# Optimization experiments

Measured on AMD Instinct MI355X. Metric: run time of the kernel, lower is better.

The kernel has to match this reference:

```python
import jax, jax.numpy as jnp
import numpy as np

MASK_VALUE = -1000000.0  # matches torch sequence_mask fill value


def setup_inputs() -> dict:
    key = jax.random.key(0)
    k1, k2, k3, k4 = jax.random.split(key, 4)
    B, Tq, Tk, d = 16, 2048, 2048, 128
    queries = jax.random.normal(k1, (B, Tq, d), dtype=jnp.float32)
    keys = jax.random.normal(k2, (B, Tk, d), dtype=jnp.float32)
    values = jax.random.normal(k3, (B, Tk, d), dtype=jnp.float32)
    valid_lens = jax.random.randint(k4, (B, Tq), 0, Tk, dtype=jnp.int64)
    return {"queries": queries, "keys": keys, "values": values,
            "valid_lens": valid_lens}


def reference(queries, keys, values, valid_lens):
    d = queries.shape[-1]
    Tk = keys.shape[1]
    # scores: [B, Tq, Tk]
    scores = jnp.einsum('bqd,bkd->bqk', queries, keys) / jnp.sqrt(
        jnp.asarray(d, dtype=queries.dtype))
    # per-row length mask: position k is valid iff k < valid_lens[b, q]
    mask = jnp.arange(Tk)[None, None, :] < valid_lens[:, :, None]
    scores = jnp.where(mask, scores, jnp.asarray(MASK_VALUE, scores.dtype))
    attn = jax.nn.softmax(scores, axis=-1)
    # dropout p=0.0 -> identity
    return jnp.einsum('bqk,bkd->bqd', attn, values)
```

## Files before the change

kernel.cpp:

```cpp
#include <hip/hip_runtime.h>
#include <stdint.h>
#include <math.h>

#define NB 16
#define TQ 2048
#define TK 2048
#define DH 128
#define KT (TK / 64)
#define QB (TQ / 64)

#define QK_STR 136
#define VT_STR 72
#define P_STR  72

typedef __attribute__((ext_vector_type(8))) short bf16x8;
typedef __attribute__((ext_vector_type(4))) float f32x4;
typedef __attribute__((ext_vector_type(8))) unsigned short u16x8;

__device__ __forceinline__ unsigned short f2b(float f) {
  union { float f; uint32_t u; } v; v.f = f;
  uint32_t u = v.u;
  return (unsigned short)((u + 0x7fffu + ((u >> 16) & 1u)) >> 16);
}

__device__ __forceinline__ u16x8 cvt8(const float* p) {
  const f32x4 a = *(const f32x4*)p;
  const f32x4 b = *(const f32x4*)(p + 4);
  u16x8 o;
#pragma unroll
  for (int j = 0; j < 4; ++j) { o[j] = f2b(a[j]); o[4 + j] = f2b(b[j]); }
  return o;
}

__global__ __launch_bounds__(256) void sort_kernel(const int* __restrict__ vlen,
                                                   int* __restrict__ perm) {
  __shared__ int cnt[TK + 1];
  __shared__ int base_[TK + 1];
  __shared__ int psum[256];
  const int b = blockIdx.x;
  const int t = threadIdx.x;

  int hw = 0;
#pragma unroll
  for (int i = 0; i < 8; ++i) hw |= vlen[2 * i + 1];
  const bool is64 = (hw == 0);

  for (int i = t; i <= TK; i += 256) cnt[i] = 0;
  __syncthreads();

  int eff[8];
#pragma unroll
  for (int j = 0; j < 8; ++j) {
    const int q = j * 256 + t;
    const int idx = b * TQ + q;
    int v = is64 ? vlen[2 * idx] : vlen[idx];
    v = (v < 0) ? 0 : ((v > TK) ? TK : v);
    eff[j] = (v == 0) ? TK : v;
    atomicAdd(&cnt[eff[j]], 1);
  }
  __syncthreads();

  int loc[8]; int s = 0;
#pragma unroll
  for (int j = 0; j < 8; ++j) { loc[j] = cnt[TK - (t * 8 + j)]; s += loc[j]; }
  psum[t] = s;
  __syncthreads();
  if (t == 0) {
    int acc = 0;
    for (int i = 0; i < 256; ++i) { const int x = psum[i]; psum[i] = acc; acc += x; }
  }
  __syncthreads();
  int run = psum[t];
#pragma unroll
  for (int j = 0; j < 8; ++j) { base_[TK - (t * 8 + j)] = run; run += loc[j]; }
  __syncthreads();
#pragma unroll
  for (int j = 0; j < 8; ++j) {
    const int rank = atomicAdd(&base_[eff[j]], 1);
    perm[b * TQ + rank] = j * 256 + t;
  }
}

__global__ __launch_bounds__(256) void prep_kernel(const float* __restrict__ K,
                                                   const float* __restrict__ V,
                                                   unsigned short* __restrict__ Kb,
                                                   unsigned short* __restrict__ Vt) {
  __shared__ alignas(16) unsigned short tile[64][136];
  const int t = threadIdx.x;
  const int b = blockIdx.y;
  const int kt = blockIdx.x;
  const int k0 = kt * 64;

  const float* Ks = K + ((size_t)b * TK + k0) * DH;
  unsigned short* Kd = Kb + ((size_t)b * TK + k0) * DH;
#pragma unroll
  for (int i = 0; i < 4; ++i) {
    const int row = i * 16 + (t >> 4);
    const int c0 = (t & 15) * 8;
    *(u16x8*)(Kd + (size_t)row * DH + c0) = cvt8(Ks + (size_t)row * DH + c0);
  }
  const float* Vs = V + ((size_t)b * TK + k0) * DH;
#pragma unroll
  for (int i = 0; i < 4; ++i) {
    const int row = i * 16 + (t >> 4);
    const int c0 = (t & 15) * 8;
    *(u16x8*)(&tile[row][c0]) = cvt8(Vs + (size_t)row * DH + c0);
  }
  __syncthreads();
  {
    const int d = t >> 1;
    const int half = t & 1;
    alignas(16) unsigned short tmp[32];
#pragma unroll
    for (int j = 0; j < 32; ++j) tmp[j] = tile[half * 32 + j][d];
    unsigned short* dst = Vt + ((size_t)(b * KT + kt) * DH + d) * 64 + half * 32;
#pragma unroll
    for (int j = 0; j < 4; ++j)
      *(u16x8*)(dst + j * 8) = *(const u16x8*)(&tmp[j * 8]);
  }
}

__global__ __launch_bounds__(256) void attn_ws(const float* __restrict__ Q,
                                               const unsigned short* __restrict__ Kp,
                                               const unsigned short* __restrict__ Vp,
                                               const int* __restrict__ vlen,
                                               const int* __restrict__ perm,
                                               float* __restrict__ pO,
                                               float* __restrict__ pL,
                                               float* __restrict__ out,
                                               const int split) {
  __shared__ alignas(16) char smem[53248];
  __shared__ int s_bvl[4];
  unsigned short* sQ = (unsigned short*)smem;
  unsigned short* sK = (unsigned short*)(smem + 17408);
  unsigned short* sV = (unsigned short*)(smem + 34816);

  const int tid  = threadIdx.x;
  const int w    = tid >> 6;
  const int lane = tid & 63;
  const int quad = lane >> 4;
  const int l15  = lane & 15;
  const int b    = blockIdx.y;
  int jq, cchunk;
  if (split) { jq = blockIdx.x >> 1; cchunk = blockIdx.x & 1; }
  else       { jq = blockIdx.x;      cchunk = 0; }
  const int q0 = jq * 64;

#pragma unroll
  for (int i = 0; i < 4; ++i) {
    const int row = i * 16 + (tid >> 4);
    const int qi = perm ? perm[b * TQ + q0 + row] : (q0 + row);
    const int c0 = (tid & 15) * 8;
    *(u16x8*)(sQ + row * QK_STR + c0) = cvt8(Q + ((size_t)b * TQ + qi) * DH + c0);
  }

  int hw = 0;
#pragma unroll
  for (int i = 0; i < 8; ++i) hw |= vlen[2 * i + 1];
  const bool is64 = (hw == 0);

  const float kScaleL2 = 0.08838834764831845f * 1.4426950408889634f;
  const float kBias    = -32.0f;
  const float kKill    = -1.0e7f;

  const int qw = q0 + w * 16;
  int vlr[4];
  float scl[4];
  int qidx[4];
#pragma unroll
  for (int r = 0; r < 4; ++r) {
    const int rank = qw + quad * 4 + r;
    const int qrow = perm ? perm[b * TQ + rank] : rank;
    qidx[r] = qrow;
    const int idx = b * TQ + qrow;
    int v = is64 ? vlen[2 * idx] : vlen[idx];
    v = (v < 0) ? 0 : ((v > TK) ? TK : v);
    scl[r] = (v == 0) ? 0.0f : kScaleL2;
    vlr[r] = (v == 0) ? TK : v;
  }
  int wvl = 0;
#pragma unroll
  for (int r = 0; r < 4; ++r) wvl = max(wvl, vlr[r]);
  wvl = max(wvl, __shfl_xor(wvl, 16, 64));
  wvl = max(wvl, __shfl_xor(wvl, 32, 64));
  if (lane == 0) s_bvl[w] = wvl;

  __syncthreads();
  const int bvl = max(max(s_bvl[0], s_bvl[1]), max(s_bvl[2], s_bvl[3]));
  const int nt = (bvl + 63) >> 6;
  int t0 = 0, t1 = nt;
  if (split) {
    const int half = (nt + 1) >> 1;
    t0 = cchunk * half;
    t1 = cchunk ? nt : half;
  }

  bf16x8 qa[4];
  {
    const unsigned short* qrow = sQ + (w * 16 + l15) * QK_STR;
#pragma unroll
    for (int kc = 0; kc < 4; ++kc)
      qa[kc] = *(const bf16x8*)(qrow + (kc * 4 + quad) * 8);
  }
  unsigned short* sP = (unsigned short*)smem + w * (16 * P_STR);

  f32x4 Of[8] = {};
  float l_r[4] = {0.f, 0.f, 0.f, 0.f};

  const unsigned short* Kbase = Kp + (size_t)b * TK * DH;
  const unsigned short* Vbase = Vp + (size_t)(b * KT) * DH * 64;
  const int krow = tid >> 4;
  const int kch  = tid & 15;

  u16x8 kreg[4], vreg[4];
  if (t0 < t1) {
    const unsigned short* Ksrc = Kbase + (size_t)t0 * 64 * DH;
#pragma unroll
    for (int i = 0; i < 4; ++i)
      kreg[i] = *(const u16x8*)(Ksrc + (size_t)(i * 16 + krow) * DH + kch * 8);
    const unsigned short* Vsrc = Vbase + (size_t)t0 * (DH * 64);
#pragma unroll
    for (int i = 0; i < 4; ++i)
      vreg[i] = *(const u16x8*)(Vsrc + (i * 256 + tid) * 8);
  }

  for (int t = t0; t < t1; ++t) {
#pragma unroll
    for (int i = 0; i < 4; ++i)
      *(u16x8*)(sK + (i * 16 + krow) * QK_STR + kch * 8) = kreg[i];
#pragma unroll
    for (int i = 0; i < 4; ++i) {
      const int chunk = i * 256 + tid;
      *(u16x8*)(sV + (chunk >> 3) * VT_STR + (chunk & 7) * 8) = vreg[i];
    }
    __syncthreads();

    if (t + 1 < t1) {
      const unsigned short* Ksrc = Kbase + (size_t)(t + 1) * 64 * DH;
#pragma unroll
      for (int i = 0; i < 4; ++i)
        kreg[i] = *(const u16x8*)(Ksrc + (size_t)(i * 16 + krow) * DH + kch * 8);
      const unsigned short* Vsrc = Vbase + (size_t)(t + 1) * (DH * 64);
#pragma unroll
      for (int i = 0; i < 4; ++i)
        vreg[i] = *(const u16x8*)(Vsrc + (i * 256 + tid) * 8);
    }

    const int k0 = t * 64;
    if (k0 < wvl) {
      f32x4 sc[4] = {};
#pragma unroll
      for (int ct = 0; ct < 4; ++ct) {
        const unsigned short* kr = sK + (ct * 16 + l15) * QK_STR;
#pragma unroll
        for (int kc = 0; kc < 4; ++kc) {
          const bf16x8 kf = *(const bf16x8*)(kr + (kc * 4 + quad) * 8);
          sc[ct] = __builtin_amdgcn_mfma_f32_16x16x32_bf16(qa[kc], kf, sc[ct], 0, 0, 0);
        }
      }

      unsigned short pb[4][4];
#pragma unroll
      for (int ct = 0; ct < 4; ++ct) {
        const int kpos = k0 + ct * 16 + l15;
#pragma unroll
        for (int r = 0; r < 4; ++r) {
          const float s = (kpos < vlr[r]) ? fmaf(sc[ct][r], scl[r], kBias) : kKill;
          const float p = exp2f(s);
          l_r[r] += p;
          pb[ct][r] = f2b(p);
        }
      }

#pragma unroll
      for (int ct = 0; ct < 4; ++ct)
#pragma unroll
        for (int r = 0; r < 4; ++r)
          sP[(quad * 4 + r) * P_STR + ct * 16 + l15] = pb[ct][r];
      __asm__ __volatile__("" ::: "memory");

      bf16x8 pa[2];
      {
        const unsigned short* pr = sP + l15 * P_STR;
#pragma unroll
        for (int ch = 0; ch < 2; ++ch)
          pa[ch] = *(const bf16x8*)(pr + (ch * 4 + quad) * 8);
      }

#pragma unroll
      for (int dt = 0; dt < 8; ++dt) {
        const unsigned short* vr = sV + (dt * 16 + l15) * VT_STR;
#pragma unroll
        for (int ch = 0; ch < 2; ++ch) {
          const bf16x8 vf = *(const bf16x8*)(vr + (ch * 4 + quad) * 8);
          Of[dt] = __builtin_amdgcn_mfma_f32_16x16x32_bf16(pa[ch], vf, Of[dt], 0, 0, 0);
        }
      }
    }
    __syncthreads();
  }

#pragma unroll
  for (int off = 1; off <= 8; off <<= 1)
#pragma unroll
    for (int r = 0; r < 4; ++r)
      l_r[r] += __shfl_xor(l_r[r], off, 64);

  if (split) {
    const int slot = (b * QB + jq) * 2 + cchunk;
    float* po = pO + (size_t)slot * (64 * DH);
    float* pl = pL + (size_t)slot * 64;
#pragma unroll
    for (int r = 0; r < 4; ++r) {
      const int row = w * 16 + quad * 4 + r;
#pragma unroll
      for (int dt = 0; dt < 8; ++dt)
        po[(size_t)row * DH + dt * 16 + l15] = Of[dt][r];
    }
    if (l15 == 0) {
#pragma unroll
      for (int r = 0; r < 4; ++r)
        pl[w * 16 + quad * 4 + r] = l_r[r];
    }
  } else {
#pragma unroll
    for (int r = 0; r < 4; ++r) {
      const float inv = 1.0f / l_r[r];
      float* orow = out + ((size_t)b * TQ + qidx[r]) * DH;
#pragma unroll
      for (int dt = 0; dt < 8; ++dt)
        orow[dt * 16 + l15] = Of[dt][r] * inv;
    }
  }
}

__global__ __launch_bounds__(256) void combine_kernel(const float* __restrict__ pO,
                                                      const float* __restrict__ pL,
                                                      const int* __restrict__ perm,
                                                      float* __restrict__ out) {
  const int b = blockIdx.y;
  const int j = blockIdx.x;
  const int t = threadIdx.x;
  const int s0 = (b * QB + j) * 2;
  const float* a0 = pO + (size_t)s0 * (64 * DH);
  const float* a1 = a0 + 64 * DH;
  const float* l0 = pL + (size_t)s0 * 64;
#pragma unroll
  for (int i = 0; i < 8; ++i) {
    const int u = i * 256 + t;
    const int r = u >> 5;
    const int d4 = (u & 31) * 4;
    const float l = l0[r] + l0[64 + r];
    const float inv = 1.0f / l;
    const f32x4 x = *(const f32x4*)(a0 + (size_t)r * DH + d4);
    const f32x4 y = *(const f32x4*)(a1 + (size_t)r * DH + d4);
    const int qi = perm[b * TQ + j * 64 + r];
    *(f32x4*)(out + ((size_t)b * TQ + qi) * DH + d4) = (x + y) * inv;
  }
}

__global__ __launch_bounds__(256) void attn_fb(const float* __restrict__ Q,
                                               const float* __restrict__ Kp,
                                               const float* __restrict__ Vp,
                                               const int* __restrict__ vlen,
                                               float* __restrict__ out) {
  __shared__ alignas(16) char smem[53248];
  __shared__ int s_bvl[4];
  unsigned short* sQ = (unsigned short*)smem;
  unsigned short* sK = (unsigned short*)(smem + 17408);
  unsigned short* sV = (unsigned short*)(smem + 34816);

  const int tid  = threadIdx.x;
  const int w    = tid >> 6;
  const int lane = tid & 63;
  const int quad = lane >> 4;
  const int l15  = lane & 15;
  const int b    = blockIdx.y;
  const int q0   = blockIdx.x * 64;

  const float* Qb = Q + ((size_t)b * TQ + q0) * DH;
#pragma unroll
  for (int i = 0; i < 4; ++i) {
    const int row = i * 16 + (tid >> 4);
    const int c0 = (tid & 15) * 8;
    *(u16x8*)(sQ + row * QK_STR + c0) = cvt8(Qb + (size_t)row * DH + c0);
  }

  int hw = 0;
#pragma unroll
  for (int i = 0; i < 8; ++i) hw |= vlen[2 * i + 1];
  const bool is64 = (hw == 0);

  const float kScaleL2 = 0.08838834764831845f * 1.4426950408889634f;
  const float kBias    = -32.0f;
  const float kKill    = -1.0e7f;

  const int qw = q0 + w * 16;
  int vlr[4];
  float scl[4];
#pragma unroll
  for (int r = 0; r < 4; ++r) {
    const int idx = b * TQ + qw + quad * 4 + r;
    int v = is64 ? vlen[2 * idx] : vlen[idx];
    v = (v < 0) ? 0 : ((v > TK) ? TK : v);
    scl[r] = (v == 0) ? 0.0f : kScaleL2;
    vlr[r] = (v == 0) ? TK : v;
  }
  int wvl = 0;
#pragma unroll
  for (int r = 0; r < 4; ++r) wvl = max(wvl, vlr[r]);
  wvl = max(wvl, __shfl_xor(wvl, 16, 64));
  wvl = max(wvl, __shfl_xor(wvl, 32, 64));
  if (lane == 0) s_bvl[w] = wvl;
  __syncthreads();
  const int bvl = max(max(s_bvl[0], s_bvl[1]), max(s_bvl[2], s_bvl[3]));
  const int nt = (bvl + 63) >> 6;

  bf16x8 qa[4];
  {
    const unsigned short* qrow = sQ + (w * 16 + l15) * QK_STR;
#pragma unroll
    for (int kc = 0; kc < 4; ++kc)
      qa[kc] = *(const bf16x8*)(qrow + (kc * 4 + quad) * 8);
  }
  unsigned short* sP = (unsigned short*)smem + w * (16 * P_STR);

  f32x4 Of[8] = {};
  float l_r[4] = {0.f, 0.f, 0.f, 0.f};

  const float* Kb = Kp + (size_t)b * TK * DH;
  const float* Vb = Vp + (size_t)b * TK * DH;

  for (int t = 0; t < nt; ++t) {
    const int k0 = t * 64;
    __syncthreads();
#pragma unroll
    for (int i = 0; i < 4; ++i) {
      const int row = i * 16 + (tid >> 4);
      const int c0 = (tid & 15) * 8;
      *(u16x8*)(sK + row * QK_STR + c0) = cvt8(Kb + (size_t)(k0 + row) * DH + c0);
    }
#pragma unroll
    for (int i = 0; i < 4; ++i) {
      const int row = i * 16 + (tid >> 4);
      const int c0 = (tid & 15) * 8;
      *(u16x8*)(sV + row * QK_STR + c0) = cvt8(Vb + (size_t)(k0 + row) * DH + c0);
    }
    __syncthreads();
    if (k0 >= wvl) continue;

    f32x4 sc[4] = {};
#pragma unroll
    for (int ct = 0; ct < 4; ++ct) {
      const unsigned short* kr = sK + (ct * 16 + l15) * QK_STR;
#pragma unroll
      for (int kc = 0; kc < 4; ++kc) {
        const bf16x8 kf = *(const bf16x8*)(kr + (kc * 4 + quad) * 8);
        sc[ct] = __builtin_amdgcn_mfma_f32_16x16x32_bf16(qa[kc], kf, sc[ct], 0, 0, 0);
      }
    }
    unsigned short pb[4][4];
#pragma unroll
    for (int ct = 0; ct < 4; ++ct) {
      const int kpos = k0 + ct * 16 + l15;
#pragma unroll
      for (int r = 0; r < 4; ++r) {
        const float s = (kpos < vlr[r]) ? fmaf(sc[ct][r], scl[r], kBias) : kKill;
        const float p = exp2f(s);
        l_r[r] += p;
        pb[ct][r] = f2b(p);
      }
    }
#pragma unroll
    for (int ct = 0; ct < 4; ++ct)
#pragma unroll
      for (int r = 0; r < 4; ++r)
        sP[(quad * 4 + r) * P_STR + ct * 16 + l15] = pb[ct][r];
    __asm__ __volatile__("" ::: "memory");
    bf16x8 pa[2];
    {
      const unsigned short* pr = sP + l15 * P_STR;
#pragma unroll
      for (int ch = 0; ch < 2; ++ch)
        pa[ch] = *(const bf16x8*)(pr + (ch * 4 + quad) * 8);
    }
#pragma unroll
    for (int dt = 0; dt < 8; ++dt) {
      const int col = dt * 16 + l15;
#pragma unroll
      for (int ch = 0; ch < 2; ++ch) {
        bf16x8 vf;
#pragma unroll
        for (int j = 0; j < 8; ++j) {
          const int k = ch * 32 + quad * 8 + j;
          vf[j] = ((const short*)sV)[k * QK_STR + col];
        }
        Of[dt] = __builtin_amdgcn_mfma_f32_16x16x32_bf16(pa[ch], vf, Of[dt], 0, 0, 0);
      }
    }
  }

#pragma unroll
  for (int off = 1; off <= 8; off <<= 1)
#pragma unroll
    for (int r = 0; r < 4; ++r)
      l_r[r] += __shfl_xor(l_r[r], off, 64);

#pragma unroll
  for (int r = 0; r < 4; ++r) {
    const float inv = 1.0f / l_r[r];
    const int q = qw + quad * 4 + r;
    float* orow = out + ((size_t)b * TQ + q) * DH;
#pragma unroll
    for (int dt = 0; dt < 8; ++dt)
      orow[dt * 16 + l15] = Of[dt][r] * inv;
  }
}

extern "C" void kernel_launch(void* const* d_in, const int* in_sizes, int n_in,
                              void* d_out, int out_size, void* d_ws, size_t ws_size,
                              hipStream_t stream) {
  const float* Q = (const float*)d_in[0];
  const float* K = (const float*)d_in[1];
  const float* V = (const float*)d_in[2];
  const int* vl  = (const int*)d_in[3];
  float* out     = (float*)d_out;

  const size_t kb    = (size_t)NB * TK * DH;
  const size_t kvB   = kb * 2 * 2;
  const size_t permB = (size_t)NB * TQ * sizeof(int);
  const size_t pLB   = (size_t)NB * QB * 2 * 64 * sizeof(float);
  const size_t pOB   = (size_t)NB * QB * 2 * 64 * DH * sizeof(float);

  if (ws_size >= kvB + permB + pLB + pOB) {
    unsigned short* Kb = (unsigned short*)d_ws;
    unsigned short* Vt = Kb + kb;
    int*   perm = (int*)((char*)d_ws + kvB);
    float* pL   = (float*)((char*)d_ws + kvB + permB);
    float* pO   = (float*)((char*)d_ws + kvB + permB + pLB);
    sort_kernel<<<dim3(NB), 256, 0, stream>>>(vl, perm);
    prep_kernel<<<dim3(KT, NB), 256, 0, stream>>>(K, V, Kb, Vt);
    attn_ws<<<dim3(QB * 2, NB), 256, 0, stream>>>(Q, Kb, Vt, vl, perm, pO, pL, out, 1);
    combine_kernel<<<dim3(QB, NB), 256, 0, stream>>>(pO, pL, perm, out);
  } else if (ws_size >= kvB + permB) {
    unsigned short* Kb = (unsigned short*)d_ws;
    unsigned short* Vt = Kb + kb;
    int* perm = (int*)((char*)d_ws + kvB);
    sort_kernel<<<dim3(NB), 256, 0, stream>>>(vl, perm);
    prep_kernel<<<dim3(KT, NB), 256, 0, stream>>>(K, V, Kb, Vt);
    attn_ws<<<dim3(QB, NB), 256, 0, stream>>>(Q, Kb, Vt, vl, perm, nullptr, nullptr, out, 0);
  } else if (ws_size >= kvB) {
    unsigned short* Kb = (unsigned short*)d_ws;
    unsigned short* Vt = Kb + kb;
    prep_kernel<<<dim3(KT, NB), 256, 0, stream>>>(K, V, Kb, Vt);
    attn_ws<<<dim3(QB, NB), 256, 0, stream>>>(Q, Kb, Vt, vl, nullptr, nullptr, nullptr, out, 0);
  } else {
    attn_fb<<<dim3(QB, NB), 256, 0, stream>>>(Q, K, V, vl, out);
  }
}
```

Measured before the change: 189.0 us.

## Split key range into fixed chunks with in-kernel last-block combine

Result: slower. 580.5 us (+207.2%).

```diff
diff --git a/kernel.cpp b/kernel.cpp
--- a/kernel.cpp
+++ b/kernel.cpp
@@ -33,19 +33,22 @@
 }
 
 __global__ __launch_bounds__(256) void sort_kernel(const int* __restrict__ vlen,
-                                                   int* __restrict__ perm) {
-  __shared__ int cnt[TK + 1];
+                                                   int* __restrict__ perm,
+                                                   int* __restrict__ cnt) {
+  __shared__ int cnt_[TK + 1];
   __shared__ int base_[TK + 1];
   __shared__ int psum[256];
   const int b = blockIdx.x;
   const int t = threadIdx.x;
 
+  if (cnt && t < QB) cnt[b * QB + t] = 0;
+
   int hw = 0;
 #pragma unroll
   for (int i = 0; i < 8; ++i) hw |= vlen[2 * i + 1];
   const bool is64 = (hw == 0);
 
-  for (int i = t; i <= TK; i += 256) cnt[i] = 0;
+  for (int i = t; i <= TK; i += 256) cnt_[i] = 0;
   __syncthreads();
 
   int eff[8];
@@ -56,13 +59,13 @@
     int v = is64 ? vlen[2 * idx] : vlen[idx];
     v = (v < 0) ? 0 : ((v > TK) ? TK : v);
     eff[j] = (v == 0) ? TK : v;
-    atomicAdd(&cnt[eff[j]], 1);
+    atomicAdd(&cnt_[eff[j]], 1);
   }
   __syncthreads();
 
   int loc[8]; int s = 0;
 #pragma unroll
-  for (int j = 0; j < 8; ++j) { loc[j] = cnt[TK - (t * 8 + j)]; s += loc[j]; }
+  for (int j = 0; j < 8; ++j) { loc[j] = cnt_[TK - (t * 8 + j)]; s += loc[j]; }
   psum[t] = s;
   __syncthreads();
   if (t == 0) {
@@ -127,10 +130,12 @@
                                                const int* __restrict__ perm,
                                                float* __restrict__ pO,
                                                float* __restrict__ pL,
+                                               int* __restrict__ cnt,
                                                float* __restrict__ out,
-                                               const int split) {
+                                               const int nchs) {
   __shared__ alignas(16) char smem[53248];
   __shared__ int s_bvl[4];
+  __shared__ int s_last;
   unsigned short* sQ = (unsigned short*)smem;
   unsigned short* sK = (unsigned short*)(smem + 17408);
   unsigned short* sV = (unsigned short*)(smem + 34816);
@@ -141,18 +146,13 @@
   const int quad = lane >> 4;
   const int l15  = lane & 15;
   const int b    = blockIdx.y;
-  int jq, cchunk;
-  if (split) { jq = blockIdx.x >> 1; cchunk = blockIdx.x & 1; }
-  else       { jq = blockIdx.x;      cchunk = 0; }
+  const int nch  = 1 << nchs;
+  const int ctl  = 5 - nchs;
+  const int ctiles = KT >> nchs;
+  const int jq     = blockIdx.x >> nchs;
+  const int cchunk = blockIdx.x & (nch - 1);
   const int q0 = jq * 64;
-
-#pragma unroll
-  for (int i = 0; i < 4; ++i) {
-    const int row = i * 16 + (tid >> 4);
-    const int qi = perm ? perm[b * TQ + q0 + row] : (q0 + row);
-    const int c0 = (tid & 15) * 8;
-    *(u16x8*)(sQ + row * QK_STR + c0) = cvt8(Q + ((size_t)b * TQ + qi) * DH + c0);
-  }
+  const int qw = q0 + w * 16;
 
   int hw = 0;
 #pragma unroll
@@ -163,10 +163,43 @@
   const float kBias    = -32.0f;
   const float kKill    = -1.0e7f;
 
-  const int qw = q0 + w * 16;
-  int vlr[4];
-  float scl[4];
-  int qidx[4];
+  int bvl, wvl;
+  if (perm) {
+    const int qb0 = perm[b * TQ + q0];
+    const int qw0 = perm[b * TQ + qw];
+    int v0 = is64 ? vlen[2 * (b * TQ + qb0)] : vlen[b * TQ + qb0];
+    int vw = is64 ? vlen[2 * (b * TQ + qw0)] : vlen[b * TQ + qw0];
+    v0 = (v0 < 0) ? 0 : ((v0 > TK) ? TK : v0);
+    vw = (vw < 0) ? 0 : ((vw > TK) ? TK : vw);
+    bvl = (v0 == 0) ? TK : v0;
+    wvl = (vw == 0) ? TK : vw;
+  } else {
+    int vlr0[4];
+#pragma unroll
+    for (int r = 0; r < 4; ++r) {
+      const int idx = b * TQ + qw + quad * 4 + r;
+      int v = is64 ? vlen[2 * idx] : vlen[idx];
+      v = (v < 0) ? 0 : ((v > TK) ? TK : v);
+      vlr0[r] = (v == 0) ? TK : v;
+    }
+    int m = 0;
+#pragma unroll
+    for (int r = 0; r < 4; ++r) m = max(m, vlr0[r]);
+    m = max(m, __shfl_xor(m, 16, 64));
+    m = max(m, __shfl_xor(m, 32, 64));
+    if (lane == 0) s_bvl[w] = m;
+    __syncthreads();
+    bvl = max(max(s_bvl[0], s_bvl[1]), max(s_bvl[2], s_bvl[3]));
+    wvl = m;
+  }
+
+  const int nt = (bvl + 63) >> 6;
+  const int t0 = cchunk * ctiles;
+  const int t1 = (nt < t0 + ctiles) ? nt : (t0 + ctiles);
+  if (t0 >= t1) return;
+  const int nact = (nt + ctiles - 1) >> ctl;
+
+  int vlr[4]; float scl[4]; int qidx[4];
 #pragma unroll
   for (int r = 0; r < 4; ++r) {
     const int rank = qw + quad * 4 + r;
@@ -178,22 +211,15 @@
     scl[r] = (v == 0) ? 0.0f : kScaleL2;
     vlr[r] = (v == 0) ? TK : v;
   }
-  int wvl = 0;
-#pragma unroll
-  for (int r = 0; r < 4; ++r) wvl = max(wvl, vlr[r]);
-  wvl = max(wvl, __shfl_xor(wvl, 16, 64));
-  wvl = max(wvl, __shfl_xor(wvl, 32, 64));
-  if (lane == 0) s_bvl[w] = wvl;
-
-  __syncthreads();
-  const int bvl = max(max(s_bvl[0], s_bvl[1]), max(s_bvl[2], s_bvl[3]));
-  const int nt = (bvl + 63) >> 6;
-  int t0 = 0, t1 = nt;
-  if (split) {
-    const int half = (nt + 1) >> 1;
-    t0 = cchunk * half;
-    t1 = cchunk ? nt : half;
-  }
+
+#pragma unroll
+  for (int i = 0; i < 4; ++i) {
+    const int row = i * 16 + (tid >> 4);
+    const int qi = perm ? perm[b * TQ + q0 + row] : (q0 + row);
+    const int c0 = (tid & 15) * 8;
+    *(u16x8*)(sQ + row * QK_STR + c0) = cvt8(Q + ((size_t)b * TQ + qi) * DH + c0);
+  }
+  __syncthreads();
 
   bf16x8 qa[4];
   {
@@ -213,7 +239,7 @@
   const int kch  = tid & 15;
 
   u16x8 kreg[4], vreg[4];
-  if (t0 < t1) {
+  {
     const unsigned short* Ksrc = Kbase + (size_t)t0 * 64 * DH;
 #pragma unroll
     for (int i = 0; i < 4; ++i)
@@ -306,23 +332,7 @@
     for (int r = 0; r < 4; ++r)
       l_r[r] += __shfl_xor(l_r[r], off, 64);
 
-  if (split) {
-    const int slot = (b * QB + jq) * 2 + cchunk;
-    float* po = pO + (size_t)slot * (64 * DH);
-    float* pl = pL + (size_t)slot * 64;
-#pragma unroll
-    for (int r = 0; r < 4; ++r) {
-      const int row = w * 16 + quad * 4 + r;
-#pragma unroll
-      for (int dt = 0; dt < 8; ++dt)
-        po[(size_t)row * DH + dt * 16 + l15] = Of[dt][r];
-    }
-    if (l15 == 0) {
-#pragma unroll
-      for (int r = 0; r < 4; ++r)
-        pl[w * 16 + quad * 4 + r] = l_r[r];
-    }
-  } else {
+  if (nact == 1) {
 #pragma unroll
     for (int r = 0; r < 4; ++r) {
       const float inv = 1.0f / l_r[r];
@@ -331,31 +341,51 @@
       for (int dt = 0; dt < 8; ++dt)
         orow[dt * 16 + l15] = Of[dt][r] * inv;
     }
-  }
-}
-
-__global__ __launch_bounds__(256) void combine_kernel(const float* __restrict__ pO,
-                                                      const float* __restrict__ pL,
-                                                      const int* __restrict__ perm,
-                                                      float* __restrict__ out) {
-  const int b = blockIdx.y;
-  const int j = blockIdx.x;
-  const int t = threadIdx.x;
-  const int s0 = (b * QB + j) * 2;
-  const float* a0 = pO + (size_t)s0 * (64 * DH);
-  const float* a1 = a0 + 64 * DH;
-  const float* l0 = pL + (size_t)s0 * 64;
+    return;
+  }
+
+  const int qb = b * QB + jq;
+  const int slot = qb * nch + cchunk;
+  {
+    float* po = pO + (size_t)slot * (64 * DH);
+    float* pl = pL + (size_t)slot * 64;
+#pragma unroll
+    for (int r = 0; r < 4; ++r) {
+      const int row = w * 16 + quad * 4 + r;
+#pragma unroll
+      for (int dt = 0; dt < 8; ++dt)
+        po[(size_t)row * DH + dt * 16 + l15] = Of[dt][r];
+    }
+    if (l15 == 0) {
+#pragma unroll
+      for (int r = 0; r < 4; ++r)
+        pl[w * 16 + quad * 4 + r] = l_r[r];
+    }
+  }
+
+  __threadfence();
+  __syncthreads();
+  if (tid == 0)
+    s_last = (atomicAdd(&cnt[qb], 1) == nact - 1) ? 1 : 0;
+  __syncthreads();
+  if (!s_last) return;
+
+  __threadfence();
+  const int qboff = qb * nch;
 #pragma unroll
   for (int i = 0; i < 8; ++i) {
-    const int u = i * 256 + t;
+    const int u = i * 256 + tid;
     const int r = u >> 5;
     const int d4 = (u & 31) * 4;
-    const float l = l0[r] + l0[64 + r];
-    const float inv = 1.0f / l;
-    const f32x4 x = *(const f32x4*)(a0 + (size_t)r * DH + d4);
-    const f32x4 y = *(const f32x4*)(a1 + (size_t)r * DH + d4);
-    const int qi = perm[b * TQ + j * 64 + r];
-    *(f32x4*)(out + ((size_t)b * TQ + qi) * DH + d4) = (x + y) * inv;
+    float lsum = 0.0f;
+    f32x4 acc = {0.f, 0.f, 0.f, 0.f};
+    for (int c = 0; c < nact; ++c) {
+      lsum += pL[(size_t)(qboff + c) * 64 + r];
+      acc += *(const f32x4*)(pO + ((size_t)(qboff + c) * 64 + r) * DH + d4);
+    }
+    const float inv = 1.0f / lsum;
+    const int qi = perm[b * TQ + q0 + r];
+    *(f32x4*)(out + ((size_t)b * TQ + qi) * DH + d4) = acc * inv;
   }
 }
 
@@ -529,31 +559,36 @@
   const size_t kb    = (size_t)NB * TK * DH;
   const size_t kvB   = kb * 2 * 2;
   const size_t permB = (size_t)NB * TQ * sizeof(int);
-  const size_t pLB   = (size_t)NB * QB * 2 * 64 * sizeof(float);
-  const size_t pOB   = (size_t)NB * QB * 2 * 64 * DH * sizeof(float);
-
-  if (ws_size >= kvB + permB + pLB + pOB) {
+  const size_t cntB  = 4096;
+  const size_t baseB = kvB + permB + cntB;
+
+  int nchs = -1;
+  size_t pLB = 0, pOB = 0;
+  for (int s = 2; s >= 0; --s) {
+    const size_t nch = (size_t)1 << s;
+    const size_t plb = (size_t)NB * QB * nch * 64 * sizeof(float);
+    const size_t pob = (size_t)NB * QB * nch * 64 * DH * sizeof(float);
+    const size_t need = (s > 0) ? (baseB + plb + pob) : (kvB + permB);
+    if (ws_size >= need) { nchs = s; pLB = plb; pOB = pob; break; }
+  }
+
+  if (nchs >= 0) {
     unsigned short* Kb = (unsigned short*)d_ws;
     unsigned short* Vt = Kb + kb;
     int*   perm = (int*)((char*)d_ws + kvB);
-    float* pL   = (float*)((char*)d_ws + kvB + permB);
-    float* pO   = (float*)((char*)d_ws + kvB + permB + pLB);
-    sort_kernel<<<dim3(NB), 256, 0, stream>>>(vl, perm);
+    int*   cnt  = (nchs > 0) ? (int*)((char*)d_ws + kvB + permB) : nullptr;
+    float* pL   = (nchs > 0) ? (float*)((char*)d_ws + baseB) : nullptr;
+    float* pO   = (nchs > 0) ? (float*)((char*)d_ws + baseB + pLB) : nullptr;
+    sort_kernel<<<dim3(NB), 256, 0, stream>>>(vl, perm, cnt);
     prep_kernel<<<dim3(KT, NB), 256, 0, stream>>>(K, V, Kb, Vt);
-    attn_ws<<<dim3(QB * 2, NB), 256, 0, stream>>>(Q, Kb, Vt, vl, perm, pO, pL, out, 1);
-    combine_kernel<<<dim3(QB, NB), 256, 0, stream>>>(pO, pL, perm, out);
-  } else if (ws_size >= kvB + permB) {
-    unsigned short* Kb = (unsigned short*)d_ws;
-    unsigned short* Vt = Kb + kb;
-    int* perm = (int*)((char*)d_ws + kvB);
-    sort_kernel<<<dim3(NB), 256, 0, stream>>>(vl, perm);
-    prep_kernel<<<dim3(KT, NB), 256, 0, stream>>>(K, V, Kb, Vt);
-    attn_ws<<<dim3(QB, NB), 256, 0, stream>>>(Q, Kb, Vt, vl, perm, nullptr, nullptr, out, 0);
+    attn_ws<<<dim3(QB << nchs, NB), 256, 0, stream>>>(Q, Kb, Vt, vl, perm,
+                                                      pO, pL, cnt, out, nchs);
   } else if (ws_size >= kvB) {
     unsigned short* Kb = (unsigned short*)d_ws;
     unsigned short* Vt = Kb + kb;
     prep_kernel<<<dim3(KT, NB), 256, 0, stream>>>(K, V, Kb, Vt);
-    attn_ws<<<dim3(QB, NB), 256, 0, stream>>>(Q, Kb, Vt, vl, nullptr, nullptr, nullptr, out, 0);
+    attn_ws<<<dim3(QB, NB), 256, 0, stream>>>(Q, Kb, Vt, vl, nullptr,
+                                              nullptr, nullptr, nullptr, out, 0);
   } else {
     attn_fb<<<dim3(QB, NB), 256, 0, stream>>>(Q, K, V, vl, out);
   }
```
